# Kernel tuning notes

Measured on AMD Instinct MI355X. Metric: run time of the kernel, lower is better.

The kernel has to match this reference:

```python
import jax, jax.numpy as jnp
import numpy as np

D_MODEL = 768

def setup_inputs() -> dict:
    key = jax.random.key(0)
    k1, k2, k3, k4 = jax.random.split(key, 4)
    x = jax.random.normal(k1, (2, 2048, D_MODEL), dtype=jnp.float32)
    w_qkv = jax.random.normal(k2, (3 * D_MODEL, D_MODEL), dtype=jnp.float32) * (1.0 / np.sqrt(D_MODEL))
    w_fc = jax.random.normal(k3, (D_MODEL, D_MODEL), dtype=jnp.float32) * (1.0 / np.sqrt(D_MODEL))
    b_fc = jax.random.normal(k4, (D_MODEL,), dtype=jnp.float32) * 0.01
    return {"x": x, "w_qkv": w_qkv, "w_fc": w_fc, "b_fc": b_fc, "n_head": 12}


def reference(x, w_qkv, w_fc, b_fc, n_head):
    b, n, d = x.shape
    h = int(n_head)
    d_k = d // h
    temperature = float(d_k) ** 0.5  # NOTE: source MULTIPLIES by sqrt(d_k)
    qkv = x @ w_qkv.T                                  # [b, n, 3d] (qkv_bias=False)
    # rearrange 'b n (qkv d h) -> qkv b h n d' : split order is (qkv, d_k, h)
    qkv = qkv.reshape(b, n, 3, d_k, h).transpose(2, 0, 4, 1, 3)  # [3, b, h, n, d_k]
    q, k, v = qkv[0], qkv[1], qkv[2]
    attn = jnp.einsum('bhid,bhjd->bhij', q, k) * temperature      # [b, h, n, n]
    attn = jax.nn.softmax(attn, axis=-1)                           # dropout p=0 -> identity
    out = jnp.einsum('bhij,bhjd->bhid', attn, v)                   # [b, h, n, d_k]
    out = out.transpose(0, 2, 1, 3).reshape(b, n, d)               # 'b h n d -> b n (h d)'
    out = out @ w_fc.T + b_fc                                      # fc (dropout p=0 -> identity)
    return out
```

## Files before the change

kernel.cpp:

```cpp
#include <hip/hip_runtime.h>
#include <stdint.h>

typedef float f32x4 __attribute__((ext_vector_type(4)));
typedef _Float16 f16;
typedef f16 f16x8 __attribute__((ext_vector_type(8)));
typedef f16 f16x4 __attribute__((ext_vector_type(4)));
typedef f16 f16x2 __attribute__((ext_vector_type(2)));

#define MFMA16(a, b, c) __builtin_amdgcn_mfma_f32_16x16x32_f16((a), (b), (c), 0, 0, 0)

__device__ __forceinline__ float fexp2(float x) {
    return __builtin_amdgcn_exp2f(x);
}
__device__ __forceinline__ f16x2 cvt_pk_f16(float a, float b) {
    auto p = __builtin_amdgcn_cvt_pkrtz(a, b);
    return *(f16x2*)&p;
}

typedef __attribute__((address_space(1))) const uint32_t gu32;
typedef __attribute__((address_space(3))) uint32_t lu32;
__device__ __forceinline__ void gload_lds16(const void* g, void* l) {
    __builtin_amdgcn_global_load_lds((gu32*)g, (lu32*)l, 16, 0, 0);
}

__device__ __forceinline__ size_t kv_elem(int bh, int n, int d) {
    const int kt = n >> 6, row = n & 63;
    return ((size_t)(bh * 32 + kt)) * 4096 + row * 64 + (((d >> 3) ^ (row & 7)) << 3) + (d & 7);
}

__global__ void split_inputs(const float* __restrict__ X, const float* __restrict__ Wq,
                             const float* __restrict__ Wf,
                             f16* __restrict__ Xh, f16* __restrict__ Xl,
                             f16* __restrict__ Wh, f16* __restrict__ Wfb) {
    const int tid = blockIdx.x * 256 + threadIdx.x;
    if (tid < 393216) {
        const float* s = X + (size_t)tid * 8;
        f16 hi[8], lo[8];
#pragma unroll
        for (int j = 0; j < 8; j += 4) {
            f32x4 v = *(const f32x4*)(s + j);
#pragma unroll
            for (int q = 0; q < 4; ++q) {
                f16 h = (f16)v[q];
                hi[j + q] = h;
                lo[j + q] = (f16)(v[q] - (float)h);
            }
        }
        *(f16x8*)(Xh + (size_t)tid * 8) = *(f16x8*)hi;
        *(f16x8*)(Xl + (size_t)tid * 8) = *(f16x8*)lo;
    } else if (tid < 614400) {
        const int t2 = tid - 393216;
        const int row = t2 / 96;
        const int k = (t2 % 96) * 8;
        const int c = row / 768;
        const int rem = row - c * 768;
        const int d = rem / 12;
        const int h2 = rem - d * 12;
        const int cp = c * 768 + h2 * 64 + d;
        const float* s = Wq + (size_t)row * 768 + k;
        f16 hi[8];
#pragma unroll
        for (int j = 0; j < 8; j += 4) {
            f32x4 v = *(const f32x4*)(s + j);
#pragma unroll
            for (int q = 0; q < 4; ++q) hi[j + q] = (f16)v[q];
        }
        *(f16x8*)(Wh + (size_t)cp * 768 + k) = *(f16x8*)hi;
    } else {
        const int t2 = tid - 614400;
        const float* s = Wf + (size_t)t2 * 8;
        f16 hi[8];
#pragma unroll
        for (int j = 0; j < 8; j += 4) {
            f32x4 v = *(const f32x4*)(s + j);
#pragma unroll
            for (int q = 0; q < 4; ++q) hi[j + q] = (f16)v[q];
        }
        *(f16x8*)(Wfb + (size_t)t2 * 8) = *(f16x8*)hi;
    }
}

__global__ __launch_bounds__(256) void qkv_gemm(
    const f16* __restrict__ Xh, const f16* __restrict__ Xl,
    const f16* __restrict__ Wh,
    f16* __restrict__ Qh, f16* __restrict__ Ql,
    f16* __restrict__ Khg, f16* __restrict__ Vb) {
    __shared__ f16 Ah[2][4096], Al[2][4096], Bh[2][4096];
    const int t = threadIdx.x;
    const int lane = t & 63, wv = t >> 6;
    const int wm = (wv >> 1) * 64, wn = (wv & 1) * 64;
    const int r = lane & 15, g = lane >> 4;
    const int bm = blockIdx.x, bn = blockIdx.y;
    const bool full = (bn < 12);

    const int lrow = lane >> 2;
    const int lk = (lane & 3) * 8;

    f32x4 acc[4][4];
#pragma unroll
    for (int i = 0; i < 4; ++i)
#pragma unroll
        for (int j = 0; j < 4; ++j) acc[i][j] = (f32x4)0.0f;

    auto stage = [&](int ksi, int buf) {
#pragma unroll
        for (int hh = 0; hh < 2; ++hh) {
            const int ii = wv * 2 + hh;
            const int grow = ii * 16 + lrow;
            const size_t ga = (size_t)(bm * 128 + grow) * 768 + ksi * 32 + lk;
            const size_t gb = (size_t)(bn * 128 + grow) * 768 + ksi * 32 + lk;
            gload_lds16(Xh + ga, &Ah[buf][ii * 512]);
            gload_lds16(Wh + gb, &Bh[buf][ii * 512]);
            if (full) gload_lds16(Xl + ga, &Al[buf][ii * 512]);
        }
    };

    stage(0, 0);
    int cur = 0;
    for (int i = 0; i < 24; ++i) {
        __syncthreads();
        if (i < 23) stage(i + 1, cur ^ 1);

        f16x8 a_h[4], b[4];
#pragma unroll
        for (int mf = 0; mf < 4; ++mf) a_h[mf] = *(f16x8*)&Ah[cur][(wm + mf * 16 + r) * 32 + g * 8];
#pragma unroll
        for (int nf = 0; nf < 4; ++nf) b[nf] = *(f16x8*)&Bh[cur][(wn + nf * 16 + r) * 32 + g * 8];
        if (full) {
            f16x8 a_l[4];
#pragma unroll
            for (int mf = 0; mf < 4; ++mf) a_l[mf] = *(f16x8*)&Al[cur][(wm + mf * 16 + r) * 32 + g * 8];
#pragma unroll
            for (int mf = 0; mf < 4; ++mf)
#pragma unroll
                for (int nf = 0; nf < 4; ++nf) {
                    acc[mf][nf] = MFMA16(a_h[mf], b[nf], acc[mf][nf]);
                    acc[mf][nf] = MFMA16(a_l[mf], b[nf], acc[mf][nf]);
                }
        } else {
#pragma unroll
            for (int mf = 0; mf < 4; ++mf)
#pragma unroll
                for (int nf = 0; nf < 4; ++nf)
                    acc[mf][nf] = MFMA16(a_h[mf], b[nf], acc[mf][nf]);
        }
        cur ^= 1;
    }

    const int comp = bn / 6;
#pragma unroll
    for (int mf = 0; mf < 4; ++mf)
#pragma unroll
        for (int nf = 0; nf < 4; ++nf) {
            const int col = bn * 128 + wn + nf * 16 + r;
            const int h = (col >> 6) % 12;
            const int d = col & 63;
#pragma unroll
            for (int v = 0; v < 4; ++v) {
                const int row = bm * 128 + wm + mf * 16 + g * 4 + v;
                const int b2 = row >> 11, n = row & 2047;
                const int bh = b2 * 12 + h;
                float val = acc[mf][nf][v];
                if (comp == 0) {
                    const size_t dest = ((size_t)bh * 2048 + n) * 64 + d;
                    val *= 11.5415603629f;
                    f16 hi = (f16)val;
                    Qh[dest] = hi;
                    Ql[dest] = (f16)(val - (float)hi);
                } else if (comp == 1) {
                    Khg[kv_elem(bh, n, d)] = (f16)val;
                } else {
                    Vb[((size_t)bh * 2048 + n) * 64 + d] = (f16)val;
                }
            }
        }
}

__global__ void v_transpose(const f16* __restrict__ Vb, f16* __restrict__ VTg) {
    __shared__ f16 Vt[64 * 72];
    const int t = threadIdx.x;
    const int tile = blockIdx.x;
    const f16* src = Vb + (size_t)tile * 4096;
    const int row = t >> 2, d0 = (t & 3) * 16;
    *(f16x8*)&Vt[row * 72 + d0]     = *(const f16x8*)(src + row * 64 + d0);
    *(f16x8*)&Vt[row * 72 + d0 + 8] = *(const f16x8*)(src + row * 64 + d0 + 8);
    __syncthreads();
    f16* dst = VTg + (size_t)tile * 4096;
#pragma unroll
    for (int it = 0; it < 2; ++it) {
        const int c = t + it * 256;
        const int kc = c >> 8;
        const int d = (c >> 2) & 63;
        const int gg = c & 3;
        const int gl = gg ^ ((d >> 1) & 3);
        f16 o[8];
#pragma unroll
        for (int j = 0; j < 8; ++j) {
            const int kv = kc * 32 + (j >> 2) * 16 + gl * 4 + (j & 3);
            o[j] = Vt[kv * 72 + d];
        }
        *(f16x8*)(dst + (size_t)c * 8) = *(f16x8*)o;
    }
}

__global__ __launch_bounds__(256) void attn_partial(
    const f16* __restrict__ Qh, const f16* __restrict__ Ql,
    const f16* __restrict__ Khg, const f16* __restrict__ VTg,
    f16* __restrict__ OP, float* __restrict__ Mst, float* __restrict__ Lst) {
    __shared__ f16 Khs[2][4096], VTs[2][4096];

    const int t = threadIdx.x;
    const int lane = t & 63, wv = t >> 6;
    const int r = lane & 15, g = lane >> 4;
    const int bid = blockIdx.x;
    const int qb = bid & 15;
    const int pb = bid >> 4;
    const int part = pb % 3;
    const int bh = pb / 3;
    const size_t headoff = (size_t)bh * 2048 * 64;
    const int q0w = qb * 128 + wv * 32;
    const int kt0 = part * 11;
    const int nt = (part == 2) ? 10 : 11;

    f16x8 qh[2][2], ql[2][2];
#pragma unroll
    for (int qf = 0; qf < 2; ++qf)
#pragma unroll
        for (int kc = 0; kc < 2; ++kc) {
            const size_t off = headoff + (size_t)(q0w + qf * 16 + r) * 64 + kc * 32 + g * 8;
            qh[qf][kc] = *(const f16x8*)(Qh + off);
            ql[qf][kc] = *(const f16x8*)(Ql + off);
        }

    f32x4 o_accT[2][4], lacc[2];
    float m_run[2] = {-1e30f, -1e30f};
#pragma unroll
    for (int qf = 0; qf < 2; ++qf) {
        lacc[qf] = (f32x4)0.0f;
#pragma unroll
        for (int df = 0; df < 4; ++df) o_accT[qf][df] = (f32x4)0.0f;
    }
    const f16x8 ones8 = {(f16)1.0f, (f16)1.0f, (f16)1.0f, (f16)1.0f,
                         (f16)1.0f, (f16)1.0f, (f16)1.0f, (f16)1.0f};

    auto stage = [&](int kt, int buf) {
        const size_t tb = ((size_t)bh * 32 + kt) * 4096;
#pragma unroll
        for (int c2 = 0; c2 < 2; ++c2) {
            const int c = wv * 2 + c2;
            const int go = c * 512 + lane * 8;
            gload_lds16(Khg + tb + go, &Khs[buf][c * 512]);
            gload_lds16(VTg + tb + go, &VTs[buf][c * 512]);
        }
    };

    stage(kt0, 0);
    int cur = 0;
    for (int i = 0; i < nt; ++i) {
        __syncthreads();
        if (i + 1 < nt) stage(kt0 + i + 1, cur ^ 1);

        f32x4 s[2][4];
#pragma unroll
        for (int qf = 0; qf < 2; ++qf)
#pragma unroll
            for (int cf = 0; cf < 4; ++cf) s[qf][cf] = (f32x4)0.0f;
#pragma unroll
        for (int kc = 0; kc < 2; ++kc) {
            f16x8 ka[4];
#pragma unroll
            for (int cf = 0; cf < 4; ++cf)
                ka[cf] = *(f16x8*)&Khs[cur][(cf * 16 + r) * 64 + (((kc * 4 + g) ^ (r & 7)) << 3)];
#pragma unroll
            for (int cf = 0; cf < 4; ++cf)
#pragma unroll
                for (int qf = 0; qf < 2; ++qf) {
                    s[qf][cf] = MFMA16(ka[cf], qh[qf][kc], s[qf][cf]);
                    s[qf][cf] = MFMA16(ka[cf], ql[qf][kc], s[qf][cf]);
                }
        }

        f16x8 pa[2][2];
#pragma unroll
        for (int qf = 0; qf < 2; ++qf) {
            float mx = -1e30f;
#pragma unroll
            for (int cf = 0; cf < 4; ++cf)
#pragma unroll
                for (int v = 0; v < 4; ++v) mx = fmaxf(mx, s[qf][cf][v]);
            mx = fmaxf(mx, __shfl_xor(mx, 16));
            mx = fmaxf(mx, __shfl_xor(mx, 32));
            if (__any(mx - m_run[qf] > 8.0f)) {
                const float mn = fmaxf(m_run[qf], mx);
                const float sc = fexp2(m_run[qf] - mn);
                m_run[qf] = mn;
                lacc[qf] *= sc;
#pragma unroll
                for (int df = 0; df < 4; ++df) o_accT[qf][df] *= sc;
            }
            const float mr = m_run[qf];
            union { f16x8 v8; f16x2 v2[4]; } pk[2];
#pragma unroll
            for (int cf = 0; cf < 4; ++cf) {
                const float p0 = fexp2(s[qf][cf][0] - mr);
                const float p1 = fexp2(s[qf][cf][1] - mr);
                const float p2 = fexp2(s[qf][cf][2] - mr);
                const float p3 = fexp2(s[qf][cf][3] - mr);
                pk[cf >> 1].v2[(cf & 1) * 2]     = cvt_pk_f16(p0, p1);
                pk[cf >> 1].v2[(cf & 1) * 2 + 1] = cvt_pk_f16(p2, p3);
            }
            pa[qf][0] = pk[0].v8;
            pa[qf][1] = pk[1].v8;
        }

#pragma unroll
        for (int kc = 0; kc < 2; ++kc) {
#pragma unroll
            for (int df = 0; df < 4; ++df) {
                f16x8 vb = *(f16x8*)&VTs[cur][kc * 2048 + (df * 16 + r) * 32 +
                                             ((g ^ ((r >> 1) & 3)) << 3)];
#pragma unroll
                for (int qf = 0; qf < 2; ++qf)
                    o_accT[qf][df] = MFMA16(vb, pa[qf][kc], o_accT[qf][df]);
            }
#pragma unroll
            for (int qf = 0; qf < 2; ++qf)
                lacc[qf] = MFMA16(ones8, pa[qf][kc], lacc[qf]);
        }
        cur ^= 1;
    }

#pragma unroll
    for (int qf = 0; qf < 2; ++qf) {
        const int n = q0w + qf * 16 + r;
        const float lq = lacc[qf][0];
        if (g == 0) {
            Mst[pb * 2048 + n] = m_run[qf];
            Lst[pb * 2048 + n] = lq;
        }
        const float linv = 1.0f / lq;
#pragma unroll
        for (int df = 0; df < 4; ++df) {
            f16 o4[4];
#pragma unroll
            for (int v = 0; v < 4; ++v) o4[v] = (f16)(o_accT[qf][df][v] * linv);
            *(f16x4*)&OP[((size_t)pb * 2048 + n) * 64 + df * 16 + g * 4] = *(f16x4*)o4;
        }
    }
}

__global__ void attn_combine(const f16* __restrict__ OP, const float* __restrict__ Mst,
                             const float* __restrict__ Lst, f16* __restrict__ AO) {
    const int tid = blockIdx.x * 256 + threadIdx.x;
    const int d4 = (tid & 15) * 4;
    const int pr = tid >> 4;
    const int bh = pr >> 11, n = pr & 2047;
    const int i0 = (bh * 3) * 2048 + n;
    const float m0 = Mst[i0], m1 = Mst[i0 + 2048], m2 = Mst[i0 + 4096];
    const float m = fmaxf(fmaxf(m0, m1), m2);
    const float c0 = __builtin_amdgcn_exp2f(m0 - m) * Lst[i0];
    const float c1 = __builtin_amdgcn_exp2f(m1 - m) * Lst[i0 + 2048];
    const float c2 = __builtin_amdgcn_exp2f(m2 - m) * Lst[i0 + 4096];
    const float inv = 1.0f / (c0 + c1 + c2);
    f16x4 o0 = *(const f16x4*)(OP + (size_t)i0 * 64 + d4);
    f16x4 o1 = *(const f16x4*)(OP + (size_t)(i0 + 2048) * 64 + d4);
    f16x4 o2 = *(const f16x4*)(OP + (size_t)(i0 + 4096) * 64 + d4);
    const int b = bh / 12, h = bh - b * 12;
    f16 out[4];
#pragma unroll
    for (int j = 0; j < 4; ++j)
        out[j] = (f16)((c0 * (float)o0[j] + c1 * (float)o1[j] + c2 * (float)o2[j]) * inv);
    *(f16x4*)(AO + ((size_t)(b * 2048 + n)) * 768 + h * 64 + d4) = *(f16x4*)out;
}

__global__ __launch_bounds__(256) void fc_gemm(const f16* __restrict__ A,
                                               const f16* __restrict__ Wfb,
                                               const float* __restrict__ bias,
                                               float* __restrict__ OUT) {
    __shared__ f16 As[64 * 64], Bs[64 * 64];
    const int t = threadIdx.x;
    const int lane = t & 63, wv = t >> 6;
    const int wm = (wv >> 1) * 32, wn = (wv & 1) * 32;
    const int r = lane & 15, g = lane >> 4;
    const int bm = blockIdx.x, bn = blockIdx.y;

    f32x4 acc[2][2];
#pragma unroll
    for (int i = 0; i < 2; ++i)
#pragma unroll
        for (int j = 0; j < 2; ++j) acc[i][j] = (f32x4)0.0f;

    const int srow = t >> 2;
    const int ssg = (t & 3) * 2;

    for (int ks = 0; ks < 768; ks += 64) {
        const f16* as = A + (size_t)(bm * 64 + srow) * 768 + ks;
        const f16* bs = Wfb + (size_t)(bn * 64 + srow) * 768 + ks;
#pragma unroll
        for (int u = 0; u < 2; ++u) {
            const int sg = ssg + u;
            const int dst = srow * 64 + ((sg ^ (srow & 7)) << 3);
            *(f16x8*)&As[dst] = *(const f16x8*)(as + sg * 8);
            *(f16x8*)&Bs[dst] = *(const f16x8*)(bs + sg * 8);
        }
        __syncthreads();

#pragma unroll
        for (int kc = 0; kc < 2; ++kc) {
            f16x8 a[2], b[2];
#pragma unroll
            for (int mf = 0; mf < 2; ++mf) {
                const int row = wm + mf * 16 + r;
                a[mf] = *(f16x8*)&As[row * 64 + (((kc * 4 + g) ^ (row & 7)) << 3)];
            }
#pragma unroll
            for (int nf = 0; nf < 2; ++nf) {
                const int row = wn + nf * 16 + r;
                b[nf] = *(f16x8*)&Bs[row * 64 + (((kc * 4 + g) ^ (row & 7)) << 3)];
            }
#pragma unroll
            for (int mf = 0; mf < 2; ++mf)
#pragma unroll
                for (int nf = 0; nf < 2; ++nf)
                    acc[mf][nf] = MFMA16(a[mf], b[nf], acc[mf][nf]);
        }
        __syncthreads();
    }

#pragma unroll
    for (int nf = 0; nf < 2; ++nf) {
        const int col = bn * 64 + wn + nf * 16 + r;
        const float bv = bias[col];
#pragma unroll
        for (int mf = 0; mf < 2; ++mf) {
            const int row = bm * 64 + wm + mf * 16 + g * 4;
#pragma unroll
            for (int v = 0; v < 4; ++v)
                OUT[(size_t)(row + v) * 768 + col] = acc[mf][nf][v] + bv;
        }
    }
}

extern "C" void kernel_launch(void* const* d_in, const int* in_sizes, int n_in,
                              void* d_out, int out_size, void* d_ws, size_t ws_size,
                              hipStream_t stream) {
    (void)in_sizes; (void)n_in; (void)out_size; (void)ws_size;
    const float* x     = (const float*)d_in[0];
    const float* w_qkv = (const float*)d_in[1];
    const float* w_fc  = (const float*)d_in[2];
    const float* b_fc  = (const float*)d_in[3];
    float* out = (float*)d_out;

    char* ws = (char*)d_ws;
    f16* Xh  = (f16*)ws;
    f16* Xl  = Xh + 3145728;
    f16* Qh  = Xl + 3145728;
    f16* Ql  = Qh + 3145728;
    f16* Khg = Ql + 3145728;
    f16* Vb  = Khg + 3145728;
    f16* VTg = Vb + 3145728;
    f16* AO  = VTg + 3145728;
    f16* Wh  = AO + 3145728;
    f16* Wfb = Wh + 1769472;
    float* Mst = (float*)(Wfb + 589824);
    float* Lst = Mst + 147456;
    f16* OP  = (f16*)(Lst + 147456);

    split_inputs<<<2688, 256, 0, stream>>>(x, w_qkv, w_fc, Xh, Xl, Wh, Wfb);
    qkv_gemm<<<dim3(32, 18), 256, 0, stream>>>(Xh, Xl, Wh, Qh, Ql, Khg, Vb);
    v_transpose<<<768, 256, 0, stream>>>(Vb, VTg);
    attn_partial<<<1152, 256, 0, stream>>>(Qh, Ql, Khg, VTg, OP, Mst, Lst);
    attn_combine<<<3072, 256, 0, stream>>>(OP, Mst, Lst, AO);
    fc_gemm<<<dim3(64, 12), 256, 0, stream>>>(AO, Wfb, b_fc, out);
}
```

Before: 147.3 us.

## Fuse V transpose into QKV GEMM epilogue and load K/V tiles directly from global

The QKV GEMM epilogue now writes V straight into the swizzled transposed tile layout, so the separate v_transpose kernel and the intermediate Vb buffer are removed. Separately, attn_partial no longer stages K and V tiles through double-buffered LDS with barriers. Each wave loads its MFMA operands directly from global memory, relying on L1/L2 caching. This removes a launch, a buffer round-trip, LDS traffic and syncs, but makes the four waves redundantly fetch the same K/V data and exposes global load latency without explicit prefetch.

Result: faster. 135.5 us (-8.0%).

```diff
diff --git a/kernel.cpp b/kernel.cpp
--- a/kernel.cpp
+++ b/kernel.cpp
@@ -84,7 +84,7 @@
     const f16* __restrict__ Xh, const f16* __restrict__ Xl,
     const f16* __restrict__ Wh,
     f16* __restrict__ Qh, f16* __restrict__ Ql,
-    f16* __restrict__ Khg, f16* __restrict__ Vb) {
+    f16* __restrict__ Khg, f16* __restrict__ VTg) {
     __shared__ f16 Ah[2][4096], Al[2][4096], Bh[2][4096];
     const int t = threadIdx.x;
     const int lane = t & 63, wv = t >> 6;
@@ -155,60 +155,43 @@
             const int col = bn * 128 + wn + nf * 16 + r;
             const int h = (col >> 6) % 12;
             const int d = col & 63;
-#pragma unroll
-            for (int v = 0; v < 4; ++v) {
-                const int row = bm * 128 + wm + mf * 16 + g * 4 + v;
-                const int b2 = row >> 11, n = row & 2047;
+            if (comp == 2) {
+                const int row0 = bm * 128 + wm + mf * 16 + g * 4;
+                const int b2 = row0 >> 11, n = row0 & 2047;
                 const int bh = b2 * 12 + h;
-                float val = acc[mf][nf][v];
-                if (comp == 0) {
-                    const size_t dest = ((size_t)bh * 2048 + n) * 64 + d;
-                    val *= 11.5415603629f;
-                    f16 hi = (f16)val;
-                    Qh[dest] = hi;
-                    Ql[dest] = (f16)(val - (float)hi);
-                } else if (comp == 1) {
-                    Khg[kv_elem(bh, n, d)] = (f16)val;
-                } else {
-                    Vb[((size_t)bh * 2048 + n) * 64 + d] = (f16)val;
+                const int tile = bh * 32 + (n >> 6);
+                const int kvl = n & 63;
+                const int kc = kvl >> 5, u = (kvl >> 4) & 1, gl = (kvl >> 2) & 3;
+                f16 o4[4];
+#pragma unroll
+                for (int v = 0; v < 4; ++v) o4[v] = (f16)acc[mf][nf][v];
+                *(f16x4*)&VTg[(size_t)tile * 4096 + kc * 2048 + d * 32 +
+                              ((gl ^ ((d >> 1) & 3)) << 3) + u * 4] = *(f16x4*)o4;
+            } else {
+#pragma unroll
+                for (int v = 0; v < 4; ++v) {
+                    const int row = bm * 128 + wm + mf * 16 + g * 4 + v;
+                    const int b2 = row >> 11, n = row & 2047;
+                    const int bh = b2 * 12 + h;
+                    float val = acc[mf][nf][v];
+                    if (comp == 0) {
+                        const size_t dest = ((size_t)bh * 2048 + n) * 64 + d;
+                        val *= 11.5415603629f;
+                        f16 hi = (f16)val;
+                        Qh[dest] = hi;
+                        Ql[dest] = (f16)(val - (float)hi);
+                    } else {
+                        Khg[kv_elem(bh, n, d)] = (f16)val;
+                    }
                 }
             }
         }
-}
-
-__global__ void v_transpose(const f16* __restrict__ Vb, f16* __restrict__ VTg) {
-    __shared__ f16 Vt[64 * 72];
-    const int t = threadIdx.x;
-    const int tile = blockIdx.x;
-    const f16* src = Vb + (size_t)tile * 4096;
-    const int row = t >> 2, d0 = (t & 3) * 16;
-    *(f16x8*)&Vt[row * 72 + d0]     = *(const f16x8*)(src + row * 64 + d0);
-    *(f16x8*)&Vt[row * 72 + d0 + 8] = *(const f16x8*)(src + row * 64 + d0 + 8);
-    __syncthreads();
-    f16* dst = VTg + (size_t)tile * 4096;
-#pragma unroll
-    for (int it = 0; it < 2; ++it) {
-        const int c = t + it * 256;
-        const int kc = c >> 8;
-        const int d = (c >> 2) & 63;
-        const int gg = c & 3;
-        const int gl = gg ^ ((d >> 1) & 3);
-        f16 o[8];
-#pragma unroll
-        for (int j = 0; j < 8; ++j) {
-            const int kv = kc * 32 + (j >> 2) * 16 + gl * 4 + (j & 3);
-            o[j] = Vt[kv * 72 + d];
-        }
-        *(f16x8*)(dst + (size_t)c * 8) = *(f16x8*)o;
-    }
 }
 
 __global__ __launch_bounds__(256) void attn_partial(
     const f16* __restrict__ Qh, const f16* __restrict__ Ql,
     const f16* __restrict__ Khg, const f16* __restrict__ VTg,
     f16* __restrict__ OP, float* __restrict__ Mst, float* __restrict__ Lst) {
-    __shared__ f16 Khs[2][4096], VTs[2][4096];
-
     const int t = threadIdx.x;
     const int lane = t & 63, wv = t >> 6;
     const int r = lane & 15, g = lane >> 4;
@@ -222,6 +205,10 @@
     const int kt0 = part * 11;
     const int nt = (part == 2) ? 10 : 11;
 
+    const int ksw0 = ((g ^ (r & 7)) << 3);
+    const int ksw1 = (((4 + g) ^ (r & 7)) << 3);
+    const int vsw = ((g ^ ((r >> 1) & 3)) << 3);
+
     f16x8 qh[2][2], ql[2][2];
 #pragma unroll
     for (int qf = 0; qf < 2; ++qf)
@@ -243,22 +230,17 @@
     const f16x8 ones8 = {(f16)1.0f, (f16)1.0f, (f16)1.0f, (f16)1.0f,
                          (f16)1.0f, (f16)1.0f, (f16)1.0f, (f16)1.0f};
 
-    auto stage = [&](int kt, int buf) {
-        const size_t tb = ((size_t)bh * 32 + kt) * 4096;
-#pragma unroll
-        for (int c2 = 0; c2 < 2; ++c2) {
-            const int c = wv * 2 + c2;
-            const int go = c * 512 + lane * 8;
-            gload_lds16(Khg + tb + go, &Khs[buf][c * 512]);
-            gload_lds16(VTg + tb + go, &VTs[buf][c * 512]);
-        }
-    };
-
-    stage(kt0, 0);
-    int cur = 0;
     for (int i = 0; i < nt; ++i) {
-        __syncthreads();
-        if (i + 1 < nt) stage(kt0 + i + 1, cur ^ 1);
+        const int kt = kt0 + i;
+        const f16* Kt = Khg + (size_t)(bh * 32 + kt) * 4096;
+        const f16* Vt = VTg + (size_t)(bh * 32 + kt) * 4096;
+
+        f16x8 ka0[4], ka1[4];
+#pragma unroll
+        for (int cf = 0; cf < 4; ++cf) {
+            ka0[cf] = *(const f16x8*)(Kt + (cf * 16 + r) * 64 + ksw0);
+            ka1[cf] = *(const f16x8*)(Kt + (cf * 16 + r) * 64 + ksw1);
+        }
 
         f32x4 s[2][4];
 #pragma unroll
@@ -266,19 +248,21 @@
 #pragma unroll
             for (int cf = 0; cf < 4; ++cf) s[qf][cf] = (f32x4)0.0f;
 #pragma unroll
-        for (int kc = 0; kc < 2; ++kc) {
-            f16x8 ka[4];
-#pragma unroll
-            for (int cf = 0; cf < 4; ++cf)
-                ka[cf] = *(f16x8*)&Khs[cur][(cf * 16 + r) * 64 + (((kc * 4 + g) ^ (r & 7)) << 3)];
-#pragma unroll
-            for (int cf = 0; cf < 4; ++cf)
-#pragma unroll
-                for (int qf = 0; qf < 2; ++qf) {
-                    s[qf][cf] = MFMA16(ka[cf], qh[qf][kc], s[qf][cf]);
-                    s[qf][cf] = MFMA16(ka[cf], ql[qf][kc], s[qf][cf]);
-                }
-        }
+        for (int cf = 0; cf < 4; ++cf)
+#pragma unroll
+            for (int qf = 0; qf < 2; ++qf) {
+                s[qf][cf] = MFMA16(ka0[cf], qh[qf][0], s[qf][cf]);
+                s[qf][cf] = MFMA16(ka0[cf], ql[qf][0], s[qf][cf]);
+                s[qf][cf] = MFMA16(ka1[cf], qh[qf][1], s[qf][cf]);
+                s[qf][cf] = MFMA16(ka1[cf], ql[qf][1], s[qf][cf]);
+            }
+
+        f16x8 vb[2][4];
+#pragma unroll
+        for (int kc = 0; kc < 2; ++kc)
+#pragma unroll
+            for (int df = 0; df < 4; ++df)
+                vb[kc][df] = *(const f16x8*)(Vt + kc * 2048 + (df * 16 + r) * 32 + vsw);
 
         f16x8 pa[2][2];
 #pragma unroll
@@ -316,18 +300,14 @@
 #pragma unroll
         for (int kc = 0; kc < 2; ++kc) {
 #pragma unroll
-            for (int df = 0; df < 4; ++df) {
-                f16x8 vb = *(f16x8*)&VTs[cur][kc * 2048 + (df * 16 + r) * 32 +
-                                             ((g ^ ((r >> 1) & 3)) << 3)];
+            for (int df = 0; df < 4; ++df)
 #pragma unroll
                 for (int qf = 0; qf < 2; ++qf)
-                    o_accT[qf][df] = MFMA16(vb, pa[qf][kc], o_accT[qf][df]);
-            }
+                    o_accT[qf][df] = MFMA16(vb[kc][df], pa[qf][kc], o_accT[qf][df]);
 #pragma unroll
             for (int qf = 0; qf < 2; ++qf)
                 lacc[qf] = MFMA16(ones8, pa[qf][kc], lacc[qf]);
         }
-        cur ^= 1;
     }
 
 #pragma unroll
@@ -457,8 +437,7 @@
     f16* Qh  = Xl + 3145728;
     f16* Ql  = Qh + 3145728;
     f16* Khg = Ql + 3145728;
-    f16* Vb  = Khg + 3145728;
-    f16* VTg = Vb + 3145728;
+    f16* VTg = Khg + 3145728;
     f16* AO  = VTg + 3145728;
     f16* Wh  = AO + 3145728;
     f16* Wfb = Wh + 1769472;
@@ -467,8 +446,7 @@
     f16* OP  = (f16*)(Lst + 147456);
 
     split_inputs<<<2688, 256, 0, stream>>>(x, w_qkv, w_fc, Xh, Xl, Wh, Wfb);
-    qkv_gemm<<<dim3(32, 18), 256, 0, stream>>>(Xh, Xl, Wh, Qh, Ql, Khg, Vb);
-    v_transpose<<<768, 256, 0, stream>>>(Vb, VTg);
+    qkv_gemm<<<dim3(32, 18), 256, 0, stream>>>(Xh, Xl, Wh, Qh, Ql, Khg, VTg);
     attn_partial<<<1152, 256, 0, stream>>>(Qh, Ql, Khg, VTg, OP, Mst, Lst);
     attn_combine<<<3072, 256, 0, stream>>>(OP, Mst, Lst, AO);
     fc_gemm<<<dim3(64, 12), 256, 0, stream>>>(AO, Wfb, b_fc, out);
```
